# Kernel optimization log

Measured on AMD Instinct MI355X. Metric: run time of the kernel, lower is better.

The kernel has to match this reference:

```python
import jax, jax.numpy as jnp
import numpy as np

# FusedConv for key '(1,1)': di=do=1, mi=mo=16, num_freq=to_order(min(1,1))=3, to_order(d)=2d+1
B, N, K = 2, 1024, 32
E = B * N * K
EDGE_DIM, MID, SUM_SPLITS = 32, 256, 1536  # mid = edge_dim*radial_mult*len(dims) = 32*2*4
MI, MO, NF, DIN, DOUT = 16, 16, 3, 3, 3
SPLIT_OFF = 256 + 256 + 256  # offsets of splits for keys (0,0),(0,1),(1,0) before (1,1)
SPLIT_SZ = NF * MI * MO  # 768


def setup_inputs() -> dict:
    key = jax.random.key(0)
    ks = jax.random.split(key, 8)
    edges = jax.random.normal(ks[0], (B, N, K, EDGE_DIM), dtype=jnp.float32)
    feats = jax.random.normal(ks[1], (B, N, K, MI, DIN), dtype=jnp.float32)
    basis = jax.random.normal(ks[2], (E, DIN, NF * DOUT), dtype=jnp.float32)
    W1 = jax.random.normal(ks[3], (EDGE_DIM, MID), dtype=jnp.float32) / np.sqrt(EDGE_DIM)
    b1 = jnp.zeros((MID,), dtype=jnp.float32)
    W2 = jax.random.normal(ks[4], (MID, MID), dtype=jnp.float32) / np.sqrt(MID)
    b2 = jnp.zeros((MID,), dtype=jnp.float32)
    W3 = jax.random.normal(ks[5], (MID, SUM_SPLITS), dtype=jnp.float32) / np.sqrt(MID)
    return {"edges": edges, "feats": feats, "basis": basis,
            "W1": W1, "b1": b1, "W2": W2, "b2": b2, "W3": W3}


def reference(edges, feats, basis, W1, b1, W2, b2, W3):
    # radial MLP: Linear -> GELU -> Linear -> GELU -> SplitLinear (no bias)
    h = jax.nn.gelu(edges @ W1 + b1, approximate=False)
    h = jax.nn.gelu(h @ W2 + b2, approximate=False)
    rp = h @ W3                                  # [B,N,K,1536]
    rp_k = rp[..., SPLIT_OFF:SPLIT_OFF + SPLIT_SZ]  # split for key '(1,1)', flat order (o,i,f)
    # rearrange '... (o i f) -> ... o i f' then view(-1, mo, mi*nf)
    rw = rp_k.reshape(E, MO, MI * NF)            # [E,16,48]
    f = feats.reshape(E, MI, DIN)                # [E,16,3]
    tmp = jnp.einsum('eid,edz->eiz', f, basis)   # [E,16,9]
    tmp = tmp.reshape(E, MI * NF, DOUT)          # [E,48,3]
    out = jnp.einsum('eoj,ejd->eod', rw, tmp)    # [E,16,3]
    return out.reshape(B, N, K, MO, DOUT)
```

## Files before the change

### kernel.cpp

```cpp
#include <hip/hip_runtime.h>


typedef __bf16 bf16x8 __attribute__((ext_vector_type(8)));
typedef __bf16 bf16x4 __attribute__((ext_vector_type(4)));
typedef float f32x4 __attribute__((ext_vector_type(4)));

#define TE 64
#define E_TOT 65536

__device__ __forceinline__ f32x4 mfma16(bf16x8 a, bf16x8 b, f32x4 c) {
    return __builtin_amdgcn_mfma_f32_16x16x32_bf16(a, b, c, 0, 0, 0);
}

__device__ __forceinline__ float gelu_f(float x) {
    float u = x * x;
    float t = x * fmaf(u, 0.10294345f, 2.3022082f);
    return x * __builtin_amdgcn_rcpf(1.0f + __builtin_amdgcn_exp2f(-t));
}

#define WS_W1F 0u
#define WS_W2F 16384u
#define WS_W3F 147456u

#define N_W1F 8192
#define N_W2F 65536
#define N_W3F 196608
#define PREP_TOT (N_W1F + N_W2F + N_W3F)
#define PREP_V  (PREP_TOT / 8)

__global__ __launch_bounds__(256) void prep_kernel(
    const float* __restrict__ W1, const float* __restrict__ W2,
    const float* __restrict__ W3,
    __bf16* __restrict__ W1F, __bf16* __restrict__ W2F,
    __bf16* __restrict__ W3F)
{
    int v = blockIdx.x * blockDim.x + threadIdx.x;
    if (v >= PREP_V) return;
    bf16x8 o8;
    if (v < (N_W1F >> 3)) {
        int t = v >> 6, rem = v & 63, q = rem >> 4, cc = rem & 15;
        int col = t * 16 + cc;
        #pragma unroll
        for (int j = 0; j < 8; ++j)
            o8[j] = (__bf16)W1[(q * 8 + j) * 256 + col];
        *(bf16x8*)(W1F + ((size_t)v << 3)) = o8;
    } else if (v < ((N_W1F + N_W2F) >> 3)) {
        int v2 = v - (N_W1F >> 3);
        int u = v2 >> 6, t = u >> 3, ks = u & 7;
        int rem = v2 & 63, q = rem >> 4, cc = rem & 15;
        int col = t * 16 + cc;
        #pragma unroll
        for (int j = 0; j < 8; ++j)
            o8[j] = (__bf16)W2[(ks * 32 + q * 8 + j) * 256 + col];
        *(bf16x8*)(W2F + ((size_t)v2 << 3)) = o8;
    } else {
        int v3 = v - ((N_W1F + N_W2F) >> 3);
        int u = v3 >> 6, t = u >> 3, ks = u & 7;
        int rem = v3 & 63, q = rem >> 4, cc = rem & 15;
        int col = t * 16 + cc;
        #pragma unroll
        for (int j = 0; j < 8; ++j)
            o8[j] = (__bf16)W3[(ks * 32 + q * 8 + j) * 1536 + 768 + col];
        *(bf16x8*)(W3F + ((size_t)v3 << 3)) = o8;
    }
}

__global__ __launch_bounds__(512, 4) void fused_kernel(
    const float* __restrict__ edges, const __bf16* __restrict__ W1F,
    const __bf16* __restrict__ W2F, const __bf16* __restrict__ W3F,
    const float* __restrict__ b1, const float* __restrict__ b2,
    const float* __restrict__ feats, const float* __restrict__ basis,
    float* __restrict__ out)
{
    __shared__ __align__(16) unsigned char smem[81920];
    unsigned char* hS   = smem;
    unsigned char* tmpS = smem + 32768;
    unsigned char* auxS = smem + 57344;
    __bf16* featsb = (__bf16*)auxS;
    __bf16* basisb = (__bf16*)(auxS + 6400);

    const int tid = threadIdx.x;
    const int w  = tid >> 6;
    const int l  = tid & 63;
    const int c  = l & 15;
    const int q  = l >> 4;
    const int wn = w & 3;
    const int mh = w >> 2;
    const int eb = blockIdx.x * TE;
    const int ebase = mh * 32;

    const f32x4 zero = {0.f, 0.f, 0.f, 0.f};

    #pragma unroll
    for (int it = 0; it < 6; ++it) {
        int idx = tid + it * 512;
        int e = idx / 48, r = idx - e * 48;
        featsb[e * 50 + r] = (__bf16)feats[(size_t)eb * 48 + idx];
    }
    #pragma unroll
    for (int it = 0; it < 4; ++it) {
        int idx = tid + it * 512;
        if (idx < 1728) basisb[idx] = (__bf16)basis[(size_t)eb * 27 + idx];
    }

    const float* er0 = edges + (size_t)(eb + ebase + c) * 32 + q * 8;
    const float* er1 = edges + (size_t)(eb + ebase + 16 + c) * 32 + q * 8;
    f32x4 e00 = *(const f32x4*)er0;
    f32x4 e01 = *(const f32x4*)(er0 + 4);
    f32x4 e10 = *(const f32x4*)er1;
    f32x4 e11 = *(const f32x4*)(er1 + 4);
    bf16x8 a0, a1;
    #pragma unroll
    for (int j = 0; j < 4; ++j) {
        a0[j] = (__bf16)e00[j]; a0[j + 4] = (__bf16)e01[j];
        a1[j] = (__bf16)e10[j]; a1[j + 4] = (__bf16)e11[j];
    }

    f32x4 acc1[2][4];
    #pragma unroll
    for (int mt = 0; mt < 2; ++mt)
        #pragma unroll
        for (int nt = 0; nt < 4; ++nt) acc1[mt][nt] = zero;

    const __bf16* W1Fw = W1F + (size_t)(wn * 4) * 512 + (size_t)l * 8;
    #pragma unroll
    for (int nt = 0; nt < 4; ++nt) {
        bf16x8 bf = *(const bf16x8*)(W1Fw + nt * 512);
        acc1[0][nt] = mfma16(a0, bf, acc1[0][nt]);
        acc1[1][nt] = mfma16(a1, bf, acc1[1][nt]);
    }
    #pragma unroll
    for (int nt = 0; nt < 4; ++nt) {
        int col = wn * 64 + nt * 16 + c;
        float bias = b1[col];
        #pragma unroll
        for (int mt = 0; mt < 2; ++mt)
            #pragma unroll
            for (int r = 0; r < 4; ++r) {
                int e = ebase + mt * 16 + q * 4 + r;
                float g = gelu_f(acc1[mt][nt][r] + bias);
                int chunk = (col >> 3) ^ (e & 7);
                *(__bf16*)(hS + e * 512 + chunk * 16 + (col & 7) * 2) = (__bf16)g;
            }
    }
    __syncthreads();

    f32x4 acc2[2][4];
    #pragma unroll
    for (int mt = 0; mt < 2; ++mt)
        #pragma unroll
        for (int nt = 0; nt < 4; ++nt) acc2[mt][nt] = zero;

    const __bf16* W2Fw = W2F + (size_t)(wn * 4) * 4096 + (size_t)l * 8;
    {
        bf16x8 bb[3][4];
        #pragma unroll
        for (int nt = 0; nt < 4; ++nt) {
            bb[0][nt] = *(const bf16x8*)(W2Fw + nt * 4096);
            bb[1][nt] = *(const bf16x8*)(W2Fw + nt * 4096 + 512);
        }
        #pragma unroll
        for (int ks = 0; ks < 8; ++ks) {
            if (ks < 6) {
                #pragma unroll
                for (int nt = 0; nt < 4; ++nt)
                    bb[(ks + 2) % 3][nt] =
                        *(const bf16x8*)(W2Fw + nt * 4096 + (ks + 2) * 512);
            }
            bf16x8 af0, af1;
            { int m = ebase + c;      int chunk = (ks * 4 + q) ^ (m & 7); af0 = *(const bf16x8*)(hS + m * 512 + chunk * 16); }
            { int m = ebase + 16 + c; int chunk = (ks * 4 + q) ^ (m & 7); af1 = *(const bf16x8*)(hS + m * 512 + chunk * 16); }
            #pragma unroll
            for (int nt = 0; nt < 4; ++nt) {
                acc2[0][nt] = mfma16(af0, bb[ks % 3][nt], acc2[0][nt]);
                acc2[1][nt] = mfma16(af1, bb[ks % 3][nt], acc2[1][nt]);
            }
        }
    }

    {
        int e = tid & 63;
        int j0 = tid >> 6;
        const __bf16* fr = featsb + e * 50;
        const __bf16* br = basisb + e * 27;
        #pragma unroll
        for (int k2 = 0; k2 < 6; ++k2) {
            int J = j0 + k2 * 8;
            int i0 = J / 3;
            int nf = J - i0 * 3;
            float f0 = (float)fr[i0 * 3 + 0];
            float f1 = (float)fr[i0 * 3 + 1];
            float f2 = (float)fr[i0 * 3 + 2];
            const __bf16* bp = br + nf * 3;
            bf16x4 v;
            #pragma unroll
            for (int d = 0; d < 3; ++d) {
                float s = f0 * (float)bp[d] + f1 * (float)bp[9 + d] + f2 * (float)bp[18 + d];
                v[d] = (__bf16)s;
            }
            v[3] = (__bf16)0.f;
            *(bf16x4*)(tmpS + J * 512 + e * 8) = v;
        }
    }
    __syncthreads();

    #pragma unroll
    for (int nt = 0; nt < 4; ++nt) {
        int col = wn * 64 + nt * 16 + c;
        float bias = b2[col];
        #pragma unroll
        for (int mt = 0; mt < 2; ++mt)
            #pragma unroll
            for (int r = 0; r < 4; ++r) {
                int e = ebase + mt * 16 + q * 4 + r;
                float g = gelu_f(acc2[mt][nt][r] + bias);
                int chunk = (col >> 3) ^ (e & 7);
                *(__bf16*)(hS + e * 512 + chunk * 16 + (col & 7) * 2) = (__bf16)g;
            }
    }

    const __bf16* W3Fl = W3F + (size_t)l * 8;
    bf16x8 pre0[3], pre1[3];
    #pragma unroll
    for (int nt = 0; nt < 3; ++nt) {
        pre0[nt] = *(const bf16x8*)(W3Fl + (size_t)((wn * 4) * 3 + nt) * 4096);
        pre1[nt] = *(const bf16x8*)(W3Fl + (size_t)((wn * 4) * 3 + nt) * 4096 + 512);
    }

    __syncthreads();

    unsigned char* rb = auxS + w * 3072;
    const int le = l & 31, hv = l >> 5;

    #pragma unroll 1
    for (int oi = 0; oi < 4; ++oi) {
        int o = wn * 4 + oi;
        const __bf16* W3Fo = W3Fl + (size_t)(o * 3) * 4096;
        f32x4 acc3[2][3];
        #pragma unroll
        for (int mt = 0; mt < 2; ++mt)
            #pragma unroll
            for (int nt = 0; nt < 3; ++nt) acc3[mt][nt] = zero;

        bf16x8 bb[3][3];
        #pragma unroll
        for (int nt = 0; nt < 3; ++nt) { bb[0][nt] = pre0[nt]; bb[1][nt] = pre1[nt]; }

        #pragma unroll
        for (int ks = 0; ks < 8; ++ks) {
            if (ks < 6) {
                #pragma unroll
                for (int nt = 0; nt < 3; ++nt)
                    bb[(ks + 2) % 3][nt] =
                        *(const bf16x8*)(W3Fo + nt * 4096 + (ks + 2) * 512);
            }
            bf16x8 af0, af1;
            { int m = ebase + c;      int chunk = (ks * 4 + q) ^ (m & 7); af0 = *(const bf16x8*)(hS + m * 512 + chunk * 16); }
            { int m = ebase + 16 + c; int chunk = (ks * 4 + q) ^ (m & 7); af1 = *(const bf16x8*)(hS + m * 512 + chunk * 16); }
            #pragma unroll
            for (int nt = 0; nt < 3; ++nt) {
                acc3[0][nt] = mfma16(af0, bb[ks % 3][nt], acc3[0][nt]);
                acc3[1][nt] = mfma16(af1, bb[ks % 3][nt], acc3[1][nt]);
            }
        }
        {
            int on = (oi < 3) ? (o + 1) : o;
            #pragma unroll
            for (int nt = 0; nt < 3; ++nt) {
                pre0[nt] = *(const bf16x8*)(W3Fl + (size_t)(on * 3 + nt) * 4096);
                pre1[nt] = *(const bf16x8*)(W3Fl + (size_t)(on * 3 + nt) * 4096 + 512);
            }
        }
        #pragma unroll
        for (int nt = 0; nt < 3; ++nt) {
            int J = nt * 16 + c;
            #pragma unroll
            for (int mt = 0; mt < 2; ++mt) {
                bf16x4 v;
                v[0] = (__bf16)acc3[mt][nt][0];
                v[1] = (__bf16)acc3[mt][nt][1];
                v[2] = (__bf16)acc3[mt][nt][2];
                v[3] = (__bf16)acc3[mt][nt][3];
                *(bf16x4*)(rb + J * 64 + (((mt * 4 + q) ^ (J & 7)) << 3)) = v;
            }
        }
        asm volatile("" ::: "memory");

        float s0 = 0.f, s1 = 0.f, s2 = 0.f;
        #pragma unroll
        for (int jj = 0; jj < 24; ++jj) {
            int J = hv * 24 + jj;
            float rv = (float)*(const __bf16*)(rb + J * 64 +
                           ((((le >> 2) ^ (J & 7)) << 3)) + (le & 3) * 2);
            bf16x4 tv = *(const bf16x4*)(tmpS + J * 512 + (ebase + le) * 8);
            s0 = fmaf(rv, (float)tv[0], s0);
            s1 = fmaf(rv, (float)tv[1], s1);
            s2 = fmaf(rv, (float)tv[2], s2);
        }
        asm volatile("" ::: "memory");
        s0 += __shfl_xor(s0, 32, 64);
        s1 += __shfl_xor(s1, 32, 64);
        s2 += __shfl_xor(s2, 32, 64);
        if (hv == 0) {
            float* op_ptr = out + (size_t)(eb + ebase + le) * 48 + o * 3;
            op_ptr[0] = s0; op_ptr[1] = s1; op_ptr[2] = s2;
        }
    }
}

extern "C" void kernel_launch(void* const* d_in, const int* in_sizes, int n_in,
                              void* d_out, int out_size, void* d_ws, size_t ws_size,
                              hipStream_t stream) {
    const float* edges = (const float*)d_in[0];
    const float* feats = (const float*)d_in[1];
    const float* basis = (const float*)d_in[2];
    const float* W1    = (const float*)d_in[3];
    const float* b1    = (const float*)d_in[4];
    const float* W2    = (const float*)d_in[5];
    const float* b2    = (const float*)d_in[6];
    const float* W3    = (const float*)d_in[7];
    float* out = (float*)d_out;

    __bf16* W1F = (__bf16*)((char*)d_ws + WS_W1F);
    __bf16* W2F = (__bf16*)((char*)d_ws + WS_W2F);
    __bf16* W3F = (__bf16*)((char*)d_ws + WS_W3F);

    prep_kernel<<<(PREP_V + 255) / 256, 256, 0, stream>>>(W1, W2, W3, W1F, W2F, W3F);
    fused_kernel<<<E_TOT / TE, 512, 0, stream>>>(edges, W1F, W2F, W3F, b1, b2,
                                                 feats, basis, out);
}
```

Before: 166.1 us.

## Swap MFMA operands in final GEMM to contract results in registers

```diff
diff --git a/kernel.cpp b/kernel.cpp
--- a/kernel.cpp
+++ b/kernel.cpp
@@ -153,27 +153,28 @@
 
     const __bf16* W2Fw = W2F + (size_t)(wn * 4) * 4096 + (size_t)l * 8;
     {
-        bf16x8 bb[3][4];
-        #pragma unroll
-        for (int nt = 0; nt < 4; ++nt) {
-            bb[0][nt] = *(const bf16x8*)(W2Fw + nt * 4096);
-            bb[1][nt] = *(const bf16x8*)(W2Fw + nt * 4096 + 512);
-        }
+        bf16x8 cb2[4], nb2[4];
+        #pragma unroll
+        for (int nt = 0; nt < 4; ++nt)
+            cb2[nt] = *(const bf16x8*)(W2Fw + nt * 4096);
         #pragma unroll
         for (int ks = 0; ks < 8; ++ks) {
-            if (ks < 6) {
+            if (ks < 7) {
                 #pragma unroll
                 for (int nt = 0; nt < 4; ++nt)
-                    bb[(ks + 2) % 3][nt] =
-                        *(const bf16x8*)(W2Fw + nt * 4096 + (ks + 2) * 512);
+                    nb2[nt] = *(const bf16x8*)(W2Fw + nt * 4096 + (ks + 1) * 512);
             }
             bf16x8 af0, af1;
             { int m = ebase + c;      int chunk = (ks * 4 + q) ^ (m & 7); af0 = *(const bf16x8*)(hS + m * 512 + chunk * 16); }
             { int m = ebase + 16 + c; int chunk = (ks * 4 + q) ^ (m & 7); af1 = *(const bf16x8*)(hS + m * 512 + chunk * 16); }
             #pragma unroll
             for (int nt = 0; nt < 4; ++nt) {
-                acc2[0][nt] = mfma16(af0, bb[ks % 3][nt], acc2[0][nt]);
-                acc2[1][nt] = mfma16(af1, bb[ks % 3][nt], acc2[1][nt]);
+                acc2[0][nt] = mfma16(af0, cb2[nt], acc2[0][nt]);
+                acc2[1][nt] = mfma16(af1, cb2[nt], acc2[1][nt]);
+            }
+            if (ks < 7) {
+                #pragma unroll
+                for (int nt = 0; nt < 4; ++nt) cb2[nt] = nb2[nt];
             }
         }
     }
@@ -220,17 +221,12 @@
     }
 
     const __bf16* W3Fl = W3F + (size_t)l * 8;
-    bf16x8 pre0[3], pre1[3];
-    #pragma unroll
-    for (int nt = 0; nt < 3; ++nt) {
-        pre0[nt] = *(const bf16x8*)(W3Fl + (size_t)((wn * 4) * 3 + nt) * 4096);
-        pre1[nt] = *(const bf16x8*)(W3Fl + (size_t)((wn * 4) * 3 + nt) * 4096 + 512);
-    }
+    bf16x8 pre[3];
+    #pragma unroll
+    for (int nt = 0; nt < 3; ++nt)
+        pre[nt] = *(const bf16x8*)(W3Fl + ((size_t)(((wn * 4) * 3 + nt) * 8) << 9));
 
     __syncthreads();
-
-    unsigned char* rb = auxS + w * 3072;
-    const int le = l & 31, hv = l >> 5;
 
     #pragma unroll 1
     for (int oi = 0; oi < 4; ++oi) {
@@ -242,68 +238,70 @@
             #pragma unroll
             for (int nt = 0; nt < 3; ++nt) acc3[mt][nt] = zero;
 
-        bf16x8 bb[3][3];
-        #pragma unroll
-        for (int nt = 0; nt < 3; ++nt) { bb[0][nt] = pre0[nt]; bb[1][nt] = pre1[nt]; }
+        bf16x8 cb[3], nb[3];
+        #pragma unroll
+        for (int nt = 0; nt < 3; ++nt) cb[nt] = pre[nt];
 
         #pragma unroll
         for (int ks = 0; ks < 8; ++ks) {
-            if (ks < 6) {
+            if (ks < 7) {
                 #pragma unroll
                 for (int nt = 0; nt < 3; ++nt)
-                    bb[(ks + 2) % 3][nt] =
-                        *(const bf16x8*)(W3Fo + nt * 4096 + (ks + 2) * 512);
+                    nb[nt] = *(const bf16x8*)(W3Fo + nt * 4096 + (ks + 1) * 512);
             }
             bf16x8 af0, af1;
             { int m = ebase + c;      int chunk = (ks * 4 + q) ^ (m & 7); af0 = *(const bf16x8*)(hS + m * 512 + chunk * 16); }
             { int m = ebase + 16 + c; int chunk = (ks * 4 + q) ^ (m & 7); af1 = *(const bf16x8*)(hS + m * 512 + chunk * 16); }
             #pragma unroll
             for (int nt = 0; nt < 3; ++nt) {
-                acc3[0][nt] = mfma16(af0, bb[ks % 3][nt], acc3[0][nt]);
-                acc3[1][nt] = mfma16(af1, bb[ks % 3][nt], acc3[1][nt]);
+                acc3[0][nt] = mfma16(cb[nt], af0, acc3[0][nt]);
+                acc3[1][nt] = mfma16(cb[nt], af1, acc3[1][nt]);
+            }
+            if (ks < 7) {
+                #pragma unroll
+                for (int nt = 0; nt < 3; ++nt) cb[nt] = nb[nt];
             }
         }
         {
             int on = (oi < 3) ? (o + 1) : o;
             #pragma unroll
-            for (int nt = 0; nt < 3; ++nt) {
-                pre0[nt] = *(const bf16x8*)(W3Fl + (size_t)(on * 3 + nt) * 4096);
-                pre1[nt] = *(const bf16x8*)(W3Fl + (size_t)(on * 3 + nt) * 4096 + 512);
-            }
-        }
-        #pragma unroll
-        for (int nt = 0; nt < 3; ++nt) {
-            int J = nt * 16 + c;
-            #pragma unroll
-            for (int mt = 0; mt < 2; ++mt) {
-                bf16x4 v;
-                v[0] = (__bf16)acc3[mt][nt][0];
-                v[1] = (__bf16)acc3[mt][nt][1];
-                v[2] = (__bf16)acc3[mt][nt][2];
-                v[3] = (__bf16)acc3[mt][nt][3];
-                *(bf16x4*)(rb + J * 64 + (((mt * 4 + q) ^ (J & 7)) << 3)) = v;
-            }
-        }
-        asm volatile("" ::: "memory");
-
-        float s0 = 0.f, s1 = 0.f, s2 = 0.f;
-        #pragma unroll
-        for (int jj = 0; jj < 24; ++jj) {
-            int J = hv * 24 + jj;
-            float rv = (float)*(const __bf16*)(rb + J * 64 +
-                           ((((le >> 2) ^ (J & 7)) << 3)) + (le & 3) * 2);
-            bf16x4 tv = *(const bf16x4*)(tmpS + J * 512 + (ebase + le) * 8);
-            s0 = fmaf(rv, (float)tv[0], s0);
-            s1 = fmaf(rv, (float)tv[1], s1);
-            s2 = fmaf(rv, (float)tv[2], s2);
-        }
-        asm volatile("" ::: "memory");
-        s0 += __shfl_xor(s0, 32, 64);
-        s1 += __shfl_xor(s1, 32, 64);
-        s2 += __shfl_xor(s2, 32, 64);
-        if (hv == 0) {
-            float* op_ptr = out + (size_t)(eb + ebase + le) * 48 + o * 3;
-            op_ptr[0] = s0; op_ptr[1] = s1; op_ptr[2] = s2;
+            for (int nt = 0; nt < 3; ++nt)
+                pre[nt] = *(const bf16x8*)(W3Fl + (size_t)(on * 3 + nt) * 4096);
+        }
+        float s[2][3];
+        #pragma unroll
+        for (int mt = 0; mt < 2; ++mt)
+            #pragma unroll
+            for (int d = 0; d < 3; ++d) s[mt][d] = 0.f;
+
+        #pragma unroll
+        for (int nt = 0; nt < 3; ++nt)
+            #pragma unroll
+            for (int r = 0; r < 4; ++r) {
+                int J = nt * 16 + q * 4 + r;
+                float rv0 = acc3[0][nt][r];
+                float rv1 = acc3[1][nt][r];
+                bf16x4 tv0 = *(const bf16x4*)(tmpS + J * 512 + (ebase + c) * 8);
+                bf16x4 tv1 = *(const bf16x4*)(tmpS + J * 512 + (ebase + 16 + c) * 8);
+                s[0][0] = fmaf(rv0, (float)tv0[0], s[0][0]);
+                s[0][1] = fmaf(rv0, (float)tv0[1], s[0][1]);
+                s[0][2] = fmaf(rv0, (float)tv0[2], s[0][2]);
+                s[1][0] = fmaf(rv1, (float)tv1[0], s[1][0]);
+                s[1][1] = fmaf(rv1, (float)tv1[1], s[1][1]);
+                s[1][2] = fmaf(rv1, (float)tv1[2], s[1][2]);
+            }
+        #pragma unroll
+        for (int mt = 0; mt < 2; ++mt)
+            #pragma unroll
+            for (int d = 0; d < 3; ++d) {
+                s[mt][d] += __shfl_xor(s[mt][d], 16, 64);
+                s[mt][d] += __shfl_xor(s[mt][d], 32, 64);
+            }
+        if (q == 0) {
+            float* op0 = out + (size_t)(eb + ebase + c) * 48 + o * 3;
+            float* op1 = out + (size_t)(eb + ebase + 16 + c) * 48 + o * 3;
+            op0[0] = s[0][0]; op0[1] = s[0][1]; op0[2] = s[0][2];
+            op1[0] = s[1][0]; op1[1] = s[1][1]; op1[2] = s[1][2];
         }
     }
 }
```

After: 263.8 us. +58.8%, slower.
